# Kernel optimization log

Hardware: AMD Instinct MI355X
Metric: run time of the kernel (lower is better)

Reference implementation:

```python
import jax, jax.numpy as jnp
import numpy as np

N_NODES = 100000
N_EDGES = 1600000
IN_FEATS = 64
HIDDEN = 64
NUM_CLASSES = 40


def setup_inputs() -> dict:
    key = jax.random.key(0)
    ks = jax.random.split(key, 8)
    x = jax.random.normal(ks[0], (N_NODES, IN_FEATS), dtype=jnp.float32)
    edge_index = jax.random.randint(ks[1], (2, N_EDGES), 0, N_NODES, dtype=jnp.int64)
    s = 1.0 / np.sqrt(IN_FEATS)
    W1_l = jax.random.uniform(ks[2], (HIDDEN, IN_FEATS), jnp.float32, -s, s)
    b1 = jnp.zeros((HIDDEN,), jnp.float32)
    W1_r = jax.random.uniform(ks[3], (HIDDEN, IN_FEATS), jnp.float32, -s, s)
    s2 = 1.0 / np.sqrt(HIDDEN)
    W2_l = jax.random.uniform(ks[4], (NUM_CLASSES, HIDDEN), jnp.float32, -s2, s2)
    b2 = jnp.zeros((NUM_CLASSES,), jnp.float32)
    W2_r = jax.random.uniform(ks[5], (NUM_CLASSES, HIDDEN), jnp.float32, -s2, s2)
    return {"x": x, "edge_index": edge_index, "W1_l": W1_l, "b1": b1,
            "W1_r": W1_r, "W2_l": W2_l, "b2": b2, "W2_r": W2_r}


def _sage_conv(x, src, dst, Wl, b, Wr, num_nodes):
    # mean aggregation of source-node features onto target nodes
    msg = x[src]                                           # [E, d] gather
    agg = jax.ops.segment_sum(msg, dst, num_segments=num_nodes)   # [N, d]
    deg = jax.ops.segment_sum(jnp.ones((src.shape[0],), x.dtype), dst,
                              num_segments=num_nodes)      # [N]
    agg = agg / jnp.maximum(deg, 1.0)[:, None]
    # out = lin_l(agg) + lin_r(x)  (PyG SAGEConv: root weight, bias on lin_l)
    return agg @ Wl.T + b + x @ Wr.T


def reference(x, edge_index, W1_l, b1, W1_r, W2_l, b2, W2_r):
    n = x.shape[0]
    src, dst = edge_index[0], edge_index[1]
    h = _sage_conv(x, src, dst, W1_l, b1, W1_r, n)
    h = jax.nn.relu(h)
    # dropout p=0.5 only active in training; reference runs eval mode (identity)
    return _sage_conv(h, src, dst, W2_l, b2, W2_r, n)
```

## Files before the change

kernel.cpp:

```cpp
#include <hip/hip_runtime.h>

#define N_NODES 100000
#define N_EDGES 1600000
#define NCLS 40
#define BIN_SH 8
#define BIN_N 256
#define NBIN ((N_NODES + BIN_N - 1) / BIN_N)
#define BINCAP 4800
#define BKBLK 256
#define BKTHR 1024
#define CHUNK (N_EDGES / BKBLK)
#define SENTINEL N_NODES
#define NN1 (N_NODES + 1)

typedef __attribute__((ext_vector_type(8))) short s8v;
typedef __attribute__((ext_vector_type(4))) float f4v;

__device__ __forceinline__ unsigned short f2bf(float f) {
    union { float f; unsigned int u; } v; v.f = f;
    unsigned int u = v.u + 0x7FFFu + ((v.u >> 16) & 1u);
    return (unsigned short)(u >> 16);
}
__device__ __forceinline__ float blo(unsigned int u) {
    union { unsigned int u; float f; } v; v.u = u << 16; return v.f;
}
__device__ __forceinline__ float bhi(unsigned int u) {
    union { unsigned int u; float f; } v; v.u = u & 0xFFFF0000u; return v.f;
}

#if __has_builtin(__builtin_amdgcn_cvt_pk_fp8_f32) && __has_builtin(__builtin_amdgcn_cvt_f32_fp8)
#define FP8_HW 1
#else
#define FP8_HW 0
#endif

__device__ __forceinline__ unsigned char enc_e4m3_sw(float f) {
    union { float f; unsigned int u; } v; v.f = f;
    unsigned int s = (v.u >> 24) & 0x80u;
    float af = fabsf(f);
    if (af >= 448.0f) return (unsigned char)(s | 0x7E);
    if (af < 0.015625f) {
        int q = (int)rintf(af * 512.0f);
        return (unsigned char)(s | (q & 7));
    }
    unsigned int n = v.u & 0x7FFFFFFFu;
    n = n + 0x7FFFFu + ((n >> 20) & 1u);
    int e = (int)(n >> 23) - 120;
    unsigned int m = (n >> 20) & 7u;
    if (e <= 0) { int q = (int)rintf(af * 512.0f); return (unsigned char)(s | (q & 7)); }
    if (e > 15) return (unsigned char)(s | 0x7E);
    return (unsigned char)(s | (e << 3) | m);
}
__device__ __forceinline__ float dec_e4m3_sw(unsigned int byte) {
    unsigned int sgn = byte >> 7, e = (byte >> 3) & 15u, m = byte & 7u;
    float mag;
    if (e) { union { unsigned int u; float f; } v; v.u = ((e + 120u) << 23) | (m << 20); mag = v.f; }
    else mag = (float)m * 0.001953125f;
    return sgn ? -mag : mag;
}

__device__ __forceinline__ unsigned int pack4_fp8(float a, float b, float c, float d) {
#if FP8_HW
    unsigned int w = __builtin_amdgcn_cvt_pk_fp8_f32(a, b, 0u, false);
    w = __builtin_amdgcn_cvt_pk_fp8_f32(c, d, w, true);
    return w;
#else
    return (unsigned int)enc_e4m3_sw(a) | ((unsigned int)enc_e4m3_sw(b) << 8) |
           ((unsigned int)enc_e4m3_sw(c) << 16) | ((unsigned int)enc_e4m3_sw(d) << 24);
#endif
}
__device__ __forceinline__ void unpack4_fp8(unsigned int w, float& a, float& b, float& c, float& d) {
#if FP8_HW
    a = __builtin_amdgcn_cvt_f32_fp8(w, 0);
    b = __builtin_amdgcn_cvt_f32_fp8(w, 1);
    c = __builtin_amdgcn_cvt_f32_fp8(w, 2);
    d = __builtin_amdgcn_cvt_f32_fp8(w, 3);
#else
    a = dec_e4m3_sw(w & 255u); b = dec_e4m3_sw((w >> 8) & 255u);
    c = dec_e4m3_sw((w >> 16) & 255u); d = dec_e4m3_sw(w >> 24);
#endif
}

__device__ __forceinline__ void acc_bf8(uint4 u, float* a) {
    a[0] += blo(u.x); a[1] += bhi(u.x);
    a[2] += blo(u.y); a[3] += bhi(u.y);
    a[4] += blo(u.z); a[5] += bhi(u.z);
    a[6] += blo(u.w); a[7] += bhi(u.w);
}
__device__ __forceinline__ void acc_fp16x(uint4 u, float* a) {
    float f0, f1, f2, f3;
    unpack4_fp8(u.x, f0, f1, f2, f3); a[0] += f0; a[1] += f1; a[2] += f2; a[3] += f3;
    unpack4_fp8(u.y, f0, f1, f2, f3); a[4] += f0; a[5] += f1; a[6] += f2; a[7] += f3;
    unpack4_fp8(u.z, f0, f1, f2, f3); a[8] += f0; a[9] += f1; a[10] += f2; a[11] += f3;
    unpack4_fp8(u.w, f0, f1, f2, f3); a[12] += f0; a[13] += f1; a[14] += f2; a[15] += f3;
}

__global__ __launch_bounds__(BKTHR) void k_bucket(
        const int* __restrict__ srcv, const int* __restrict__ dstv,
        int* __restrict__ bcur, int* __restrict__ bedges) {
    __shared__ int cnt4[4][NBIN];
    __shared__ int base[NBIN], lcur[NBIN];
    for (int i = threadIdx.x; i < 4 * NBIN; i += BKTHR) cnt4[i / NBIN][i % NBIN] = 0;
    __syncthreads();
    const int grp = threadIdx.x >> 8;
    const int beg = blockIdx.x * CHUNK;
    const int end = beg + CHUNK;
    for (int e = beg + threadIdx.x; e < end; e += BKTHR) {
        int d = dstv[e]; d = min(max(d, 0), N_NODES - 1);
        atomicAdd(&cnt4[grp][d >> BIN_SH], 1);
    }
    __syncthreads();
    for (int i = threadIdx.x; i < NBIN; i += BKTHR) {
        int c = cnt4[0][i] + cnt4[1][i] + cnt4[2][i] + cnt4[3][i];
        base[i] = atomicAdd(&bcur[i], c);
        lcur[i] = 0;
    }
    __syncthreads();
    for (int e = beg + threadIdx.x; e < end; e += BKTHR) {
        int d = dstv[e]; d = min(max(d, 0), N_NODES - 1);
        int s = srcv[e]; s = min(max(s, 0), N_NODES - 1);
        int b = d >> BIN_SH;
        int slot = atomicAdd(&lcur[b], 1) + base[b];
        if (slot < BINCAP) bedges[b * BINCAP + slot] = ((d & (BIN_N - 1)) << 17) | s;
    }
}

__global__ __launch_bounds__(256) void k_csrfill(
        const int* __restrict__ bcur, const int* __restrict__ bedges,
        int* __restrict__ gcnt, uint2* __restrict__ offdeg,
        int* __restrict__ srcs) {
    __shared__ int dcnt[BIN_N];
    __shared__ int s[BIN_N];
    __shared__ int base_s;
    const int b = blockIdx.x;
    dcnt[threadIdx.x] = 0;
    __syncthreads();
    const int cnt = min(bcur[b], BINCAP);
    for (int e = threadIdx.x; e < cnt; e += 256)
        atomicAdd(&dcnt[bedges[b * BINCAP + e] >> 17], 1);
    __syncthreads();
    int v = dcnt[threadIdx.x];
    int pv = (v + 3) & ~3;
    s[threadIdx.x] = pv;
    __syncthreads();
    int acc = pv;
    for (int off = 1; off < 256; off <<= 1) {
        int t = (threadIdx.x >= off) ? s[threadIdx.x - off] : 0;
        __syncthreads();
        acc += t;
        s[threadIdx.x] = acc;
        __syncthreads();
    }
    if (threadIdx.x == 255) base_s = atomicAdd(gcnt, acc);
    __syncthreads();
    const int gbeg = (acc - pv) + base_s;
    const int node = (b << BIN_SH) + threadIdx.x;
    if (node < N_NODES) offdeg[node] = make_uint2((unsigned)gbeg, (unsigned)v);
    s[threadIdx.x] = gbeg;
    dcnt[threadIdx.x] = 0;
    __syncthreads();
    for (int e = threadIdx.x; e < cnt; e += 256) {
        int val = bedges[b * BINCAP + e];
        int dl = val >> 17;
        int sv = val & 0x1FFFF;
        int slot = atomicAdd(&dcnt[dl], 1);
        srcs[s[dl] + slot] = sv;
    }
    for (int p = v; p < pv; ++p) srcs[gbeg + p] = SENTINEL;
}

__global__ void k_xb(const float* __restrict__ x, unsigned int* __restrict__ xbs,
                     unsigned int* __restrict__ h2f8) {
    int i = blockIdx.x * blockDim.x + threadIdx.x;
    int stride = gridDim.x * blockDim.x;
    const int total = N_NODES * 8;
    for (int tt = i; tt < total; tt += stride) {
        int node = tt >> 3, sub = tt & 7;
        int slice = sub >> 1, half = sub & 1;
        float4 v0 = ((const float4*)x)[tt * 2];
        float4 v1 = ((const float4*)x)[tt * 2 + 1];
        uint4 o;
        o.x = (unsigned)f2bf(v0.x) | ((unsigned)f2bf(v0.y) << 16);
        o.y = (unsigned)f2bf(v0.z) | ((unsigned)f2bf(v0.w) << 16);
        o.z = (unsigned)f2bf(v1.x) | ((unsigned)f2bf(v1.y) << 16);
        o.w = (unsigned)f2bf(v1.z) | ((unsigned)f2bf(v1.w) << 16);
        ((uint4*)xbs)[((size_t)slice * NN1 + node) * 2 + half] = o;
    }
    uint4 z; z.x = 0u; z.y = 0u; z.z = 0u; z.w = 0u;
    if (i < 8) {
        int slice = i >> 1, half = i & 1;
        ((uint4*)xbs)[((size_t)slice * NN1 + N_NODES) * 2 + half] = z;
    }
    if (i >= 16 && i < 28) h2f8[(size_t)N_NODES * 16 + (i - 16)] = 0u;
}

__global__ __launch_bounds__(256) void k_agg(
        const uint2* __restrict__ offdeg, const int* __restrict__ srcs,
        const unsigned short* __restrict__ xbs, unsigned short* __restrict__ aggs) {
    const int lane = threadIdx.x & 63;
    const int w = threadIdx.x >> 6;
    const int g = lane >> 3;
    const int c = (lane >> 1) & 3;
    const int t = lane & 1;
    const int slice = (blockIdx.x & 7) >> 1;
    const int cid = ((blockIdx.x >> 3) << 1) | (blockIdx.x & 1);
    const size_t sb = (size_t)slice * NN1;
    for (int nb = (cid * 4 + w) * 8; nb < N_NODES; nb += 16384) {
        const int node = nb + g;
        uint2 od = offdeg[node];
        const int beg = (int)od.x;
        const int m = ((int)od.y + 3) >> 2;
        float a[8] = {0.f, 0.f, 0.f, 0.f, 0.f, 0.f, 0.f, 0.f};
        int j = c;
        if (j < m) {
            int4 sv = *(const int4*)&srcs[beg + 4 * j];
            while (true) {
                const int4 cur = sv;
                const int jn = j + 4;
                if (jn < m) sv = *(const int4*)&srcs[beg + 4 * jn];
                uint4 u0 = *(const uint4*)&xbs[(sb + cur.x) * 16 + t * 8];
                uint4 u1 = *(const uint4*)&xbs[(sb + cur.y) * 16 + t * 8];
                uint4 u2 = *(const uint4*)&xbs[(sb + cur.z) * 16 + t * 8];
                uint4 u3 = *(const uint4*)&xbs[(sb + cur.w) * 16 + t * 8];
                acc_bf8(u0, a); acc_bf8(u1, a); acc_bf8(u2, a); acc_bf8(u3, a);
                if (jn >= m) break;
                j = jn;
            }
        }
        #pragma unroll
        for (int k = 0; k < 8; ++k) {
            a[k] += __shfl_xor(a[k], 2, 64);
            a[k] += __shfl_xor(a[k], 4, 64);
        }
        if (c == 0) {
            float rd = 1.0f / fmaxf((float)od.y, 1.0f);
            uint4 r;
            r.x = (unsigned)f2bf(a[0] * rd) | ((unsigned)f2bf(a[1] * rd) << 16);
            r.y = (unsigned)f2bf(a[2] * rd) | ((unsigned)f2bf(a[3] * rd) << 16);
            r.z = (unsigned)f2bf(a[4] * rd) | ((unsigned)f2bf(a[5] * rd) << 16);
            r.w = (unsigned)f2bf(a[6] * rd) | ((unsigned)f2bf(a[7] * rd) << 16);
            *(uint4*)&aggs[(sb + node) * 16 + t * 8] = r;
        }
    }
}

__global__ __launch_bounds__(256) void k_dense(
        const unsigned short* __restrict__ aggs, const unsigned short* __restrict__ xbs,
        const float* __restrict__ W1l, const float* __restrict__ b1,
        const float* __restrict__ W1r,
        const float* __restrict__ W2l, const float* __restrict__ b2,
        const float* __restrict__ W2r,
        unsigned int* __restrict__ h2f8, float* __restrict__ op) {
    __shared__ __align__(16) unsigned short wl1[64][72], wr1[64][72];
    __shared__ __align__(16) unsigned short wl2[48][72], wr2[48][72];
    __shared__ __align__(16) unsigned short hsm[4][16][72];
    for (int idx = threadIdx.x; idx < 64 * 64; idx += 256) {
        int f = idx >> 6, k = idx & 63;
        wl1[f][k] = f2bf(W1l[idx]);
        wr1[f][k] = f2bf(W1r[idx]);
    }
    for (int idx = threadIdx.x; idx < 48 * 64; idx += 256) {
        int c = idx >> 6, k = idx & 63;
        wl2[c][k] = (c < NCLS) ? f2bf(W2l[c * 64 + k]) : (unsigned short)0;
        wr2[c][k] = (c < NCLS) ? f2bf(W2r[c * 64 + k]) : (unsigned short)0;
    }
    __syncthreads();
    const int w   = threadIdx.x >> 6;
    const int l15 = threadIdx.x & 15;
    const int g   = (threadIdx.x >> 4) & 3;
    const size_t sLo = (size_t)(g >> 1) * NN1;
    const size_t sHi = (size_t)(2 + (g >> 1)) * NN1;
    const int off = (g & 1) * 8;
    float b1v[4][4], b2v[3][4];
    #pragma unroll
    for (int ft = 0; ft < 4; ++ft)
        #pragma unroll
        for (int r = 0; r < 4; ++r)
            b1v[ft][r] = b1[16 * ft + 4 * g + r];
    #pragma unroll
    for (int ct = 0; ct < 3; ++ct)
        #pragma unroll
        for (int r = 0; r < 4; ++r) {
            int c = 16 * ct + 4 * g + r;
            b2v[ct][r] = (c < NCLS) ? b2[c] : 0.0f;
        }
    unsigned short* hs = &hsm[w][0][0];
    const int gw = blockIdx.x * 4 + w;
    const int nw = gridDim.x * 4;
    for (int tile = gw; tile < N_NODES / 16; tile += nw) {
        const size_t node = (size_t)tile * 16 + l15;
        s8v aB0 = *(const s8v*)&aggs[(sLo + node) * 16 + off];
        s8v aB1 = *(const s8v*)&aggs[(sHi + node) * 16 + off];
        s8v xB0 = *(const s8v*)&xbs[(sLo + node) * 16 + off];
        s8v xB1 = *(const s8v*)&xbs[(sHi + node) * 16 + off];
        #pragma unroll
        for (int ft = 0; ft < 4; ++ft) {
            f4v c;
            c[0] = b1v[ft][0]; c[1] = b1v[ft][1]; c[2] = b1v[ft][2]; c[3] = b1v[ft][3];
            const size_t rb = (size_t)(16 * ft + l15) * 144 + 16 * g;
            s8v A0 = *(const s8v*)((const char*)wl1 + rb);
            s8v A1 = *(const s8v*)((const char*)wl1 + rb + 64);
            s8v R0 = *(const s8v*)((const char*)wr1 + rb);
            s8v R1 = *(const s8v*)((const char*)wr1 + rb + 64);
            c = __builtin_amdgcn_mfma_f32_16x16x32_bf16(A0, aB0, c, 0, 0, 0);
            c = __builtin_amdgcn_mfma_f32_16x16x32_bf16(A1, aB1, c, 0, 0, 0);
            c = __builtin_amdgcn_mfma_f32_16x16x32_bf16(R0, xB0, c, 0, 0, 0);
            c = __builtin_amdgcn_mfma_f32_16x16x32_bf16(R1, xB1, c, 0, 0, 0);
            uint2 u;
            u.x = (unsigned)f2bf(fmaxf(c[0], 0.0f)) | ((unsigned)f2bf(fmaxf(c[1], 0.0f)) << 16);
            u.y = (unsigned)f2bf(fmaxf(c[2], 0.0f)) | ((unsigned)f2bf(fmaxf(c[3], 0.0f)) << 16);
            *(uint2*)((char*)hs + l15 * 144 + 32 * ft + 8 * g) = u;
        }
        s8v hB0 = *(const s8v*)((const char*)hs + l15 * 144 + 16 * g);
        s8v hB1 = *(const s8v*)((const char*)hs + l15 * 144 + 64 + 16 * g);
        #pragma unroll
        for (int ct = 0; ct < 3; ++ct) {
            f4v p; p[0] = 0.0f; p[1] = 0.0f; p[2] = 0.0f; p[3] = 0.0f;
            f4v qv;
            qv[0] = b2v[ct][0]; qv[1] = b2v[ct][1]; qv[2] = b2v[ct][2]; qv[3] = b2v[ct][3];
            const size_t rb = (size_t)(16 * ct + l15) * 144 + 16 * g;
            s8v L0 = *(const s8v*)((const char*)wl2 + rb);
            s8v L1 = *(const s8v*)((const char*)wl2 + rb + 64);
            s8v Q0 = *(const s8v*)((const char*)wr2 + rb);
            s8v Q1 = *(const s8v*)((const char*)wr2 + rb + 64);
            p  = __builtin_amdgcn_mfma_f32_16x16x32_bf16(L0, hB0, p, 0, 0, 0);
            p  = __builtin_amdgcn_mfma_f32_16x16x32_bf16(L1, hB1, p, 0, 0, 0);
            qv = __builtin_amdgcn_mfma_f32_16x16x32_bf16(Q0, hB0, qv, 0, 0, 0);
            qv = __builtin_amdgcn_mfma_f32_16x16x32_bf16(Q1, hB1, qv, 0, 0, 0);
            int c0 = 16 * ct + 4 * g;
            h2f8[node * 16 + (4 * ct + g)] = pack4_fp8(p[0], p[1], p[2], p[3]);
            if (c0 < NCLS) {
                float4 o; o.x = qv[0]; o.y = qv[1]; o.z = qv[2]; o.w = qv[3];
                *(float4*)&op[node * NCLS + c0] = o;
            }
        }
    }
}

__global__ __launch_bounds__(256) void k_out(
        const uint2* __restrict__ offdeg, const int* __restrict__ srcs,
        const unsigned int* __restrict__ h2f8, float* __restrict__ out) {
    const int lane = threadIdx.x & 63;
    const int w = threadIdx.x >> 6;
    const int g = lane >> 4;
    const int q = (lane >> 2) & 3;
    const int t = lane & 3;
    const int wid = blockIdx.x * 4 + w;
    for (int nb = wid * 4; nb < N_NODES; nb += 32768) {
        const int node = nb + g;
        uint2 od = offdeg[node];
        const int beg = (int)od.x;
        const int m = ((int)od.y + 3) >> 2;
        float a[16] = {0.f, 0.f, 0.f, 0.f, 0.f, 0.f, 0.f, 0.f,
                       0.f, 0.f, 0.f, 0.f, 0.f, 0.f, 0.f, 0.f};
        if (t < 3) {
            int j = q;
            if (j < m) {
                int4 sv = *(const int4*)&srcs[beg + 4 * j];
                while (true) {
                    const int4 cur = sv;
                    const int jn = j + 4;
                    if (jn < m) sv = *(const int4*)&srcs[beg + 4 * jn];
                    uint4 u0 = *(const uint4*)&h2f8[(size_t)cur.x * 16 + t * 4];
                    uint4 u1 = *(const uint4*)&h2f8[(size_t)cur.y * 16 + t * 4];
                    uint4 u2 = *(const uint4*)&h2f8[(size_t)cur.z * 16 + t * 4];
                    uint4 u3 = *(const uint4*)&h2f8[(size_t)cur.w * 16 + t * 4];
                    acc_fp16x(u0, a); acc_fp16x(u1, a);
                    acc_fp16x(u2, a); acc_fp16x(u3, a);
                    if (jn >= m) break;
                    j = jn;
                }
            }
        }
        #pragma unroll
        for (int k = 0; k < 16; ++k) {
            a[k] += __shfl_xor(a[k], 4, 64);
            a[k] += __shfl_xor(a[k], 8, 64);
        }
        if (q == 0 && t < 3) {
            float rd = 1.0f / fmaxf((float)od.y, 1.0f);
            const int base = t * 16;
            const int nwords = (t == 2) ? 2 : 4;
            #pragma unroll
            for (int i = 0; i < 4; ++i) {
                if (i < nwords) {
                    float4 o = *(float4*)&out[(size_t)node * NCLS + base + 4 * i];
                    o.x = fmaf(a[4 * i + 0], rd, o.x);
                    o.y = fmaf(a[4 * i + 1], rd, o.y);
                    o.z = fmaf(a[4 * i + 2], rd, o.z);
                    o.w = fmaf(a[4 * i + 3], rd, o.w);
                    *(float4*)&out[(size_t)node * NCLS + base + 4 * i] = o;
                }
            }
        }
    }
}

extern "C" void kernel_launch(void* const* d_in, const int* in_sizes, int n_in,
                              void* d_out, int out_size, void* d_ws, size_t ws_size,
                              hipStream_t stream) {
    const float* x   = (const float*)d_in[0];
    const int*   ei  = (const int*)d_in[1];
    const float* W1l = (const float*)d_in[2];
    const float* b1  = (const float*)d_in[3];
    const float* W1r = (const float*)d_in[4];
    const float* W2l = (const float*)d_in[5];
    const float* b2  = (const float*)d_in[6];
    const float* W2r = (const float*)d_in[7];
    float* out = (float*)d_out;

    const int* srcv = ei;
    const int* dstv = ei + N_EDGES;

    int* bcur   = (int*)d_ws;
    int* gcnt   = bcur + 508;
    uint2* offdeg = (uint2*)(bcur + 512);
    int* bedges = (int*)(offdeg + N_NODES);
    int* srcs   = bedges + (size_t)NBIN * BINCAP;
    unsigned short* aggs = (unsigned short*)(srcs + (size_t)N_EDGES + 3 * N_NODES + 16);
    unsigned short* xbs  = aggs + (size_t)64 * NN1;
    unsigned int*   h2f8 = (unsigned int*)(xbs + (size_t)64 * NN1);

    hipMemsetAsync(bcur, 0, 512 * sizeof(int), stream);
    k_bucket<<<BKBLK, BKTHR, 0, stream>>>(srcv, dstv, bcur, bedges);
    k_xb<<<2048, 256, 0, stream>>>(x, (unsigned int*)xbs, h2f8);
    k_csrfill<<<NBIN, 256, 0, stream>>>(bcur, bedges, gcnt, offdeg, srcs);
    k_agg<<<2048, 256, 0, stream>>>(offdeg, srcs, xbs, aggs);
    k_dense<<<768, 256, 0, stream>>>(aggs, xbs, W1l, b1, W1r, W2l, b2, W2r, h2f8, out);
    k_out<<<2048, 256, 0, stream>>>(offdeg, srcs, h2f8, out);
}
```

Measured before the change: 139.7 us.

## Gather layer-1 features from an FP8 copy and use packed FP8 decode

k_xb now also writes an FP8 e4m3 copy of x. k_agg gathers neighbor rows from that copy instead of the sliced bf16 layout, with a new lane mapping that covers a full 64-wide row per node group of 16 lanes. Both gather kernels decode through the packed cvt_pk_f32_fp8 builtin into float2 accumulators. The aim is to halve the random-gather traffic of the first aggregation and cut conversion instructions. The costs are an extra FP8 write pass, more workspace, and lower precision on the layer-1 aggregated features.

```diff
diff --git a/kernel.cpp b/kernel.cpp
--- a/kernel.cpp
+++ b/kernel.cpp
@@ -15,6 +15,7 @@
 
 typedef __attribute__((ext_vector_type(8))) short s8v;
 typedef __attribute__((ext_vector_type(4))) float f4v;
+typedef __attribute__((ext_vector_type(2))) float f2v;
 
 __device__ __forceinline__ unsigned short f2bf(float f) {
     union { float f; unsigned int u; } v; v.f = f;
@@ -32,6 +33,11 @@
 #define FP8_HW 1
 #else
 #define FP8_HW 0
+#endif
+#if __has_builtin(__builtin_amdgcn_cvt_pk_f32_fp8)
+#define FP8_PK 1
+#else
+#define FP8_PK 0
 #endif
 
 __device__ __forceinline__ unsigned char enc_e4m3_sw(float f) {
@@ -69,30 +75,21 @@
            ((unsigned int)enc_e4m3_sw(c) << 16) | ((unsigned int)enc_e4m3_sw(d) << 24);
 #endif
 }
-__device__ __forceinline__ void unpack4_fp8(unsigned int w, float& a, float& b, float& c, float& d) {
-#if FP8_HW
-    a = __builtin_amdgcn_cvt_f32_fp8(w, 0);
-    b = __builtin_amdgcn_cvt_f32_fp8(w, 1);
-    c = __builtin_amdgcn_cvt_f32_fp8(w, 2);
-    d = __builtin_amdgcn_cvt_f32_fp8(w, 3);
+
+__device__ __forceinline__ void acc_fp8pk(unsigned int w, f2v* a) {
+#if FP8_PK
+    a[0] += __builtin_amdgcn_cvt_pk_f32_fp8((int)w, false);
+    a[1] += __builtin_amdgcn_cvt_pk_f32_fp8((int)w, true);
 #else
-    a = dec_e4m3_sw(w & 255u); b = dec_e4m3_sw((w >> 8) & 255u);
-    c = dec_e4m3_sw((w >> 16) & 255u); d = dec_e4m3_sw(w >> 24);
+    f2v lo, hi;
+    lo.x = dec_e4m3_sw(w & 255u);         lo.y = dec_e4m3_sw((w >> 8) & 255u);
+    hi.x = dec_e4m3_sw((w >> 16) & 255u); hi.y = dec_e4m3_sw(w >> 24);
+    a[0] += lo; a[1] += hi;
 #endif
 }
-
-__device__ __forceinline__ void acc_bf8(uint4 u, float* a) {
-    a[0] += blo(u.x); a[1] += bhi(u.x);
-    a[2] += blo(u.y); a[3] += bhi(u.y);
-    a[4] += blo(u.z); a[5] += bhi(u.z);
-    a[6] += blo(u.w); a[7] += bhi(u.w);
-}
-__device__ __forceinline__ void acc_fp16x(uint4 u, float* a) {
-    float f0, f1, f2, f3;
-    unpack4_fp8(u.x, f0, f1, f2, f3); a[0] += f0; a[1] += f1; a[2] += f2; a[3] += f3;
-    unpack4_fp8(u.y, f0, f1, f2, f3); a[4] += f0; a[5] += f1; a[6] += f2; a[7] += f3;
-    unpack4_fp8(u.z, f0, f1, f2, f3); a[8] += f0; a[9] += f1; a[10] += f2; a[11] += f3;
-    unpack4_fp8(u.w, f0, f1, f2, f3); a[12] += f0; a[13] += f1; a[14] += f2; a[15] += f3;
+__device__ __forceinline__ void acc_fp8x16(uint4 u, f2v* a) {
+    acc_fp8pk(u.x, a + 0); acc_fp8pk(u.y, a + 2);
+    acc_fp8pk(u.z, a + 4); acc_fp8pk(u.w, a + 6);
 }
 
 __global__ __launch_bounds__(BKTHR) void k_bucket(
@@ -170,7 +167,7 @@
 }
 
 __global__ void k_xb(const float* __restrict__ x, unsigned int* __restrict__ xbs,
-                     unsigned int* __restrict__ h2f8) {
+                     unsigned int* __restrict__ h2f8, unsigned int* __restrict__ xf8) {
     int i = blockIdx.x * blockDim.x + threadIdx.x;
     int stride = gridDim.x * blockDim.x;
     const int total = N_NODES * 8;
@@ -185,6 +182,10 @@
         o.z = (unsigned)f2bf(v1.x) | ((unsigned)f2bf(v1.y) << 16);
         o.w = (unsigned)f2bf(v1.z) | ((unsigned)f2bf(v1.w) << 16);
         ((uint4*)xbs)[((size_t)slice * NN1 + node) * 2 + half] = o;
+        uint2 p;
+        p.x = pack4_fp8(v0.x, v0.y, v0.z, v0.w);
+        p.y = pack4_fp8(v1.x, v1.y, v1.z, v1.w);
+        ((uint2*)xf8)[(size_t)node * 8 + sub] = p;
     }
     uint4 z; z.x = 0u; z.y = 0u; z.z = 0u; z.w = 0u;
     if (i < 8) {
@@ -192,25 +193,26 @@
         ((uint4*)xbs)[((size_t)slice * NN1 + N_NODES) * 2 + half] = z;
     }
     if (i >= 16 && i < 28) h2f8[(size_t)N_NODES * 16 + (i - 16)] = 0u;
+    if (i >= 32 && i < 48) xf8[(size_t)N_NODES * 16 + (i - 32)] = 0u;
 }
 
 __global__ __launch_bounds__(256) void k_agg(
         const uint2* __restrict__ offdeg, const int* __restrict__ srcs,
-        const unsigned short* __restrict__ xbs, unsigned short* __restrict__ aggs) {
+        const unsigned int* __restrict__ xf8, unsigned short* __restrict__ aggs) {
     const int lane = threadIdx.x & 63;
     const int w = threadIdx.x >> 6;
-    const int g = lane >> 3;
-    const int c = (lane >> 1) & 3;
-    const int t = lane & 1;
-    const int slice = (blockIdx.x & 7) >> 1;
-    const int cid = ((blockIdx.x >> 3) << 1) | (blockIdx.x & 1);
-    const size_t sb = (size_t)slice * NN1;
-    for (int nb = (cid * 4 + w) * 8; nb < N_NODES; nb += 16384) {
+    const int g = lane >> 4;
+    const int c = (lane >> 2) & 3;
+    const int t = lane & 3;
+    const int wid = blockIdx.x * 4 + w;
+    for (int nb = wid * 4; nb < N_NODES; nb += 32768) {
         const int node = nb + g;
         uint2 od = offdeg[node];
         const int beg = (int)od.x;
         const int m = ((int)od.y + 3) >> 2;
-        float a[8] = {0.f, 0.f, 0.f, 0.f, 0.f, 0.f, 0.f, 0.f};
+        f2v a2[8];
+        #pragma unroll
+        for (int k = 0; k < 8; ++k) { a2[k].x = 0.0f; a2[k].y = 0.0f; }
         int j = c;
         if (j < m) {
             int4 sv = *(const int4*)&srcs[beg + 4 * j];
@@ -218,28 +220,36 @@
                 const int4 cur = sv;
                 const int jn = j + 4;
                 if (jn < m) sv = *(const int4*)&srcs[beg + 4 * jn];
-                uint4 u0 = *(const uint4*)&xbs[(sb + cur.x) * 16 + t * 8];
-                uint4 u1 = *(const uint4*)&xbs[(sb + cur.y) * 16 + t * 8];
-                uint4 u2 = *(const uint4*)&xbs[(sb + cur.z) * 16 + t * 8];
-                uint4 u3 = *(const uint4*)&xbs[(sb + cur.w) * 16 + t * 8];
-                acc_bf8(u0, a); acc_bf8(u1, a); acc_bf8(u2, a); acc_bf8(u3, a);
+                uint4 u0 = *(const uint4*)&xf8[(size_t)cur.x * 16 + t * 4];
+                uint4 u1 = *(const uint4*)&xf8[(size_t)cur.y * 16 + t * 4];
+                uint4 u2 = *(const uint4*)&xf8[(size_t)cur.z * 16 + t * 4];
+                uint4 u3 = *(const uint4*)&xf8[(size_t)cur.w * 16 + t * 4];
+                acc_fp8x16(u0, a2); acc_fp8x16(u1, a2);
+                acc_fp8x16(u2, a2); acc_fp8x16(u3, a2);
                 if (jn >= m) break;
                 j = jn;
             }
         }
-        #pragma unroll
-        for (int k = 0; k < 8; ++k) {
-            a[k] += __shfl_xor(a[k], 2, 64);
-            a[k] += __shfl_xor(a[k], 4, 64);
+        float* af = (float*)a2;
+        #pragma unroll
+        for (int k = 0; k < 16; ++k) {
+            af[k] += __shfl_xor(af[k], 4, 64);
+            af[k] += __shfl_xor(af[k], 8, 64);
         }
         if (c == 0) {
             float rd = 1.0f / fmaxf((float)od.y, 1.0f);
-            uint4 r;
-            r.x = (unsigned)f2bf(a[0] * rd) | ((unsigned)f2bf(a[1] * rd) << 16);
-            r.y = (unsigned)f2bf(a[2] * rd) | ((unsigned)f2bf(a[3] * rd) << 16);
-            r.z = (unsigned)f2bf(a[4] * rd) | ((unsigned)f2bf(a[5] * rd) << 16);
-            r.w = (unsigned)f2bf(a[6] * rd) | ((unsigned)f2bf(a[7] * rd) << 16);
-            *(uint4*)&aggs[(sb + node) * 16 + t * 8] = r;
+            uint4 r0, r1;
+            r0.x = (unsigned)f2bf(af[0] * rd)  | ((unsigned)f2bf(af[1] * rd) << 16);
+            r0.y = (unsigned)f2bf(af[2] * rd)  | ((unsigned)f2bf(af[3] * rd) << 16);
+            r0.z = (unsigned)f2bf(af[4] * rd)  | ((unsigned)f2bf(af[5] * rd) << 16);
+            r0.w = (unsigned)f2bf(af[6] * rd)  | ((unsigned)f2bf(af[7] * rd) << 16);
+            r1.x = (unsigned)f2bf(af[8] * rd)  | ((unsigned)f2bf(af[9] * rd) << 16);
+            r1.y = (unsigned)f2bf(af[10] * rd) | ((unsigned)f2bf(af[11] * rd) << 16);
+            r1.z = (unsigned)f2bf(af[12] * rd) | ((unsigned)f2bf(af[13] * rd) << 16);
+            r1.w = (unsigned)f2bf(af[14] * rd) | ((unsigned)f2bf(af[15] * rd) << 16);
+            unsigned short* dst = &aggs[((size_t)t * NN1 + node) * 16];
+            *(uint4*)dst = r0;
+            *(uint4*)(dst + 8) = r1;
         }
     }
 }
@@ -351,8 +361,9 @@
         uint2 od = offdeg[node];
         const int beg = (int)od.x;
         const int m = ((int)od.y + 3) >> 2;
-        float a[16] = {0.f, 0.f, 0.f, 0.f, 0.f, 0.f, 0.f, 0.f,
-                       0.f, 0.f, 0.f, 0.f, 0.f, 0.f, 0.f, 0.f};
+        f2v a2[8];
+        #pragma unroll
+        for (int k = 0; k < 8; ++k) { a2[k].x = 0.0f; a2[k].y = 0.0f; }
         if (t < 3) {
             int j = q;
             if (j < m) {
@@ -365,13 +376,14 @@
                     uint4 u1 = *(const uint4*)&h2f8[(size_t)cur.y * 16 + t * 4];
                     uint4 u2 = *(const uint4*)&h2f8[(size_t)cur.z * 16 + t * 4];
                     uint4 u3 = *(const uint4*)&h2f8[(size_t)cur.w * 16 + t * 4];
-                    acc_fp16x(u0, a); acc_fp16x(u1, a);
-                    acc_fp16x(u2, a); acc_fp16x(u3, a);
+                    acc_fp8x16(u0, a2); acc_fp8x16(u1, a2);
+                    acc_fp8x16(u2, a2); acc_fp8x16(u3, a2);
                     if (jn >= m) break;
                     j = jn;
                 }
             }
         }
+        float* a = (float*)a2;
         #pragma unroll
         for (int k = 0; k < 16; ++k) {
             a[k] += __shfl_xor(a[k], 4, 64);
@@ -420,12 +432,13 @@
     unsigned short* aggs = (unsigned short*)(srcs + (size_t)N_EDGES + 3 * N_NODES + 16);
     unsigned short* xbs  = aggs + (size_t)64 * NN1;
     unsigned int*   h2f8 = (unsigned int*)(xbs + (size_t)64 * NN1);
+    unsigned int*   xf8  = h2f8 + (size_t)16 * NN1;
 
     hipMemsetAsync(bcur, 0, 512 * sizeof(int), stream);
     k_bucket<<<BKBLK, BKTHR, 0, stream>>>(srcv, dstv, bcur, bedges);
-    k_xb<<<2048, 256, 0, stream>>>(x, (unsigned int*)xbs, h2f8);
+    k_xb<<<2048, 256, 0, stream>>>(x, (unsigned int*)xbs, h2f8, xf8);
     k_csrfill<<<NBIN, 256, 0, stream>>>(bcur, bedges, gcnt, offdeg, srcs);
-    k_agg<<<2048, 256, 0, stream>>>(offdeg, srcs, xbs, aggs);
+    k_agg<<<2048, 256, 0, stream>>>(offdeg, srcs, xf8, aggs);
     k_dense<<<768, 256, 0, stream>>>(aggs, xbs, W1l, b1, W1r, W2l, b2, W2r, h2f8, out);
     k_out<<<2048, 256, 0, stream>>>(offdeg, srcs, h2f8, out);
 }
```

After: 124.2 us. 11.0% less time.
